# Kernel optimization log

Measured on AMD Instinct MI355X. Metric: run time of the kernel, lower is better.

## Reference

```python
import jax, jax.numpy as jnp
import numpy as np

BANDS = 6
WIN = 10
STRIDE = 2
EPS_LOG = 1e-6


def _radial_masks(win, bands):
    lin = jnp.linspace(-1.0, 1.0, win)
    yy, xx = jnp.meshgrid(lin, lin, indexing='ij')
    rr = jnp.sqrt(xx * xx + yy * yy)
    rr = rr / jnp.maximum(rr.max(), 1e-6)
    edges = jnp.linspace(0.0, 1.0, bands + 1)
    masks = ((rr[None] >= edges[:-1, None, None]) & (rr[None] < edges[1:, None, None])).astype(jnp.float32)
    counts = jnp.maximum(masks.sum(axis=(-2, -1)), 1.0)  # (bands,)
    return masks, counts


def setup_inputs() -> dict:
    key = jax.random.key(0)
    x = jax.random.normal(key, (32, 3, 256, 256), dtype=jnp.float32)
    return {"x": x}


def reference(x):
    # RGB -> gray (B,1,H,W)
    gray = 0.2989 * x[:, 0:1] + 0.587 * x[:, 1:2] + 0.114 * x[:, 2:3]
    patches = jax.lax.conv_general_dilated_patches(
        gray, (WIN, WIN), (STRIDE, STRIDE), 'VALID')
    B = patches.shape[0]
    Ho, Wo = patches.shape[2], patches.shape[3]
    p = patches.reshape(B, WIN, WIN, Ho, Wo)  # (B, wy, wx, Ho, Wo)
    # Per-patch 2D FFT (ortho), fftshift, magnitude
    amp = jnp.abs(jnp.fft.fftshift(jnp.fft.fft2(p, axes=(1, 2), norm='ortho'), axes=(1, 2)))
    masks, counts = _radial_masks(WIN, BANDS)
    # One fused contraction over all bands instead of per-band masked passes
    stat = jnp.einsum('byxhw,kyx->bkhw', amp, masks) / counts[None, :, None, None]
    return jnp.log10(stat + EPS_LOG)  # (B, bands, Ho, Wo)
```

## Files before the change

kernel.cpp:

```cpp
#include <hip/hip_runtime.h>

#define HO 124
#define WO 124

typedef float f2 __attribute__((ext_vector_type(2)));
static __device__ __forceinline__ f2 fma2(f2 a, f2 b, f2 c) {
  return __builtin_elementwise_fma(a, b, c);
}
#define FSQRT(x) __builtin_amdgcn_sqrtf(x)
#define FLOG10(x) (0.30102999566398120f * __builtin_amdgcn_logf(x))

constexpr float K1 = 0.80901699437494745f;
constexpr float K2 = 0.30901699437494742f;
constexpr float G1 = 0.58778525229247314f;
constexpr float G2 = 0.95105651629515357f;

struct Tbl { float v[360]; };
constexpr Tbl mk_wv() {
  Tbl t{};
  int band[100] = {};
  int cnt[6] = {0, 0, 0, 0, 0, 0};
  for (int i = 0; i < 10; ++i)
    for (int j = 0; j < 10; ++j) {
      const int u = (2 * i - 9) < 0 ? (9 - 2 * i) : (2 * i - 9);
      const int v = (2 * j - 9) < 0 ? (9 - 2 * j) : (2 * j - 9);
      const int m = 2 * (u * u + v * v);
      int b = -1;
      for (int k = 0; k < 6; ++k)
        if (m >= 9 * k * k && m < 9 * (k + 1) * (k + 1)) b = k;
      if (u == 3 && v == 3) b = (i == 6 && j == 6) ? 2 : 1;
      if (m == 324) b = 5;
      band[i * 10 + j] = b;
      if (b >= 0) cnt[b]++;
    }
  for (int ky = 0; ky < 6; ++ky)
    for (int kx = 0; kx < 10; ++kx)
      for (int b = 0; b < 6; ++b) {
        float w = 0.0f;
        const int sp = ((ky + 5) % 10) * 10 + (kx + 5) % 10;
        if (band[sp] == b) w += 0.1f / (float)cnt[b];
        if (ky >= 1 && ky <= 4) {
          const int sp2 = ((15 - ky) % 10) * 10 + (15 - kx) % 10;
          if (band[sp2] == b) w += 0.1f / (float)cnt[b];
        }
        t.v[(ky * 10 + kx) * 6 + b] = w;
      }
  return t;
}
constexpr Tbl WVT = mk_wv();

template <int CELL, int B>
struct AccwStep {
  static __device__ __forceinline__ void run(const float amp, float* acc) {
    constexpr float w = WVT.v[CELL * 6 + B];
    if constexpr (w != 0.0f) acc[B] = fmaf(amp, w, acc[B]);
    AccwStep<CELL, B + 1>::run(amp, acc);
  }
};
template <int CELL>
struct AccwStep<CELL, 6> {
  static __device__ __forceinline__ void run(const float, float*) {}
};
template <int C1, int C2, int B>
struct Accw2Step {
  static __device__ __forceinline__ void run(const float amp, float* acc) {
    constexpr float w = WVT.v[C1 * 6 + B] + WVT.v[C2 * 6 + B];
    if constexpr (w != 0.0f) acc[B] = fmaf(amp, w, acc[B]);
    Accw2Step<C1, C2, B + 1>::run(amp, acc);
  }
};
template <int C1, int C2>
struct Accw2Step<C1, C2, 6> {
  static __device__ __forceinline__ void run(const float, float*) {}
};
#define ACCW(cell, amp) AccwStep<(cell), 0>::run((amp), acc)
#define ACCW2(c1, c2, amp) Accw2Step<(c1), (c2), 0>::run((amp), acc)

template <int KY>
__device__ __forceinline__ void plane_body(const f2* __restrict__ tbc,
                                           float* acc) {
  f2 T_[10];
#pragma unroll
  for (int q = 0; q < 10; ++q) T_[q] = tbc[q];
  const f2 EE = T_[0] + T_[5], FF = T_[0] - T_[5];
  const f2 PQ1 = T_[1] + T_[9], MN1 = T_[1] - T_[9];
  const f2 PQ2 = T_[2] + T_[8], MN2 = T_[2] - T_[8];
  const f2 PQ3 = T_[3] + T_[7], MN3 = T_[3] - T_[7];
  const f2 PQ4 = T_[4] + T_[6], MN4 = T_[4] - T_[6];
  const f2 UU1 = PQ1 - PQ4, UU2 = PQ2 - PQ3;
  const f2 VV1 = PQ1 + PQ4, VV2 = PQ2 + PQ3;
  const f2 WW1 = MN1 + MN4, WW2 = MN2 + MN3;
  const f2 ZZ1 = MN1 - MN4, ZZ2 = MN2 - MN3;
  {
    const f2 AC = EE + VV1 + VV2;
    ACCW(KY * 10 + 0, FSQRT(fmaf(AC.x, AC.x, AC.y * AC.y)));
  }
  {
    const f2 AC = FF - UU1 + UU2;
    ACCW(KY * 10 + 5, FSQRT(fmaf(AC.x, AC.x, AC.y * AC.y)));
  }
#define CPLX_PAIR(kx, AC_, DB_)                                         \
  {                                                                     \
    const f2 AC = (AC_);                                                \
    const f2 DB = (DB_);                                                \
    {                                                                   \
      const float fr = AC.x + DB.y, fi = AC.y - DB.x;                   \
      ACCW(KY * 10 + (kx), FSQRT(fmaf(fr, fr, fi * fi)));               \
    }                                                                   \
    {                                                                   \
      const float fr = AC.x - DB.y, fi = AC.y + DB.x;                   \
      ACCW(KY * 10 + 10 - (kx), FSQRT(fmaf(fr, fr, fi * fi)));          \
    }                                                                   \
  }
  CPLX_PAIR(1,
            fma2(UU1, (f2){K1, K1}, fma2(UU2, (f2){K2, K2}, FF)),
            fma2(WW1, (f2){G1, G1}, WW2 * (f2){G2, G2}));
  CPLX_PAIR(2,
            fma2(VV1, (f2){K2, K2}, fma2(VV2, (f2){-K1, -K1}, EE)),
            fma2(ZZ1, (f2){G2, G2}, ZZ2 * (f2){G1, G1}));
  CPLX_PAIR(3,
            fma2(UU1, (f2){-K2, -K2}, fma2(UU2, (f2){-K1, -K1}, FF)),
            fma2(WW1, (f2){G2, G2}, WW2 * (f2){-G1, -G1}));
  CPLX_PAIR(4,
            fma2(VV1, (f2){-K1, -K1}, fma2(VV2, (f2){K2, K2}, EE)),
            fma2(ZZ1, (f2){G1, G1}, ZZ2 * (f2){-G2, -G2}));
#undef CPLX_PAIR
}

__global__ __launch_bounds__(256, 5) void lfs_main(const float* __restrict__ x,
                                                   float* __restrict__ out) {
  __shared__ __attribute__((aligned(16))) float tile[40 * 40];
  __shared__ __attribute__((aligned(16))) f2 Tcp[4 * 16 * 40];
  __shared__ __attribute__((aligned(16))) f2 Trr2[16 * 40];
  const int tid = threadIdx.x;
  const int bx = blockIdx.x, by = blockIdx.y, bb = blockIdx.z;

  const int oy0 = by * 32, ox0 = bx * 32;
  const float* xr = x + (size_t)bb * 3 * 65536;
  const float* xg = xr + 65536;
  const float* xb = xr + 131072;
  const bool xfull = (bx < 7);
  {
    const int r0 = tid / 10, c0 = tid % 10;
    const int gy0 = oy0 + r0;
    const bool p1 = (tid < 144);
    const int t1 = tid + 256;
    const int r1 = t1 / 10, c1 = t1 % 10;
    const int gy1 = oy0 + r1;
    float4 a0 = make_float4(0.f, 0.f, 0.f, 0.f), b0 = a0, d0 = a0;
    float4 a1 = make_float4(0.f, 0.f, 0.f, 0.f), b1 = a1, d1 = a1;
    if (gy0 < 256 && (c0 < 8 || xfull)) {
      const int off = gy0 * 256 + ox0 + c0 * 4;
      a0 = *reinterpret_cast<const float4*>(xr + off);
      b0 = *reinterpret_cast<const float4*>(xg + off);
      d0 = *reinterpret_cast<const float4*>(xb + off);
    }
    if (p1 && gy1 < 256 && (c1 < 8 || xfull)) {
      const int off = gy1 * 256 + ox0 + c1 * 4;
      a1 = *reinterpret_cast<const float4*>(xr + off);
      b1 = *reinterpret_cast<const float4*>(xg + off);
      d1 = *reinterpret_cast<const float4*>(xb + off);
    }
    float4 g0, g1;
    g0.x = fmaf(0.2989f, a0.x, fmaf(0.587f, b0.x, 0.114f * d0.x));
    g0.y = fmaf(0.2989f, a0.y, fmaf(0.587f, b0.y, 0.114f * d0.y));
    g0.z = fmaf(0.2989f, a0.z, fmaf(0.587f, b0.z, 0.114f * d0.z));
    g0.w = fmaf(0.2989f, a0.w, fmaf(0.587f, b0.w, 0.114f * d0.w));
    g1.x = fmaf(0.2989f, a1.x, fmaf(0.587f, b1.x, 0.114f * d1.x));
    g1.y = fmaf(0.2989f, a1.y, fmaf(0.587f, b1.y, 0.114f * d1.y));
    g1.z = fmaf(0.2989f, a1.z, fmaf(0.587f, b1.z, 0.114f * d1.z));
    g1.w = fmaf(0.2989f, a1.w, fmaf(0.587f, b1.w, 0.114f * d1.w));
    *reinterpret_cast<float4*>(&tile[r0 * 40 + c0 * 4]) = g0;
    if (p1) *reinterpret_cast<float4*>(&tile[r1 * 40 + c1 * 4]) = g1;
  }
  __syncthreads();

  for (int a = tid; a < 320; a += 256) {
    const int r = a / 20, cp = a % 20;
    const float* tb0 = &tile[(2 * r) * 40 + 2 * cp];
    f2 col[10];
#pragma unroll
    for (int y = 0; y < 10; ++y)
      col[y] = *reinterpret_cast<const f2*>(&tb0[y * 40]);
    const f2 E = col[0] + col[5], F = col[0] - col[5];
    const f2 P1 = col[1] + col[9], M1 = col[1] - col[9];
    const f2 P2 = col[2] + col[8], M2 = col[2] - col[8];
    const f2 P3 = col[3] + col[7], M3 = col[3] - col[7];
    const f2 P4 = col[4] + col[6], M4 = col[4] - col[6];
    const f2 U1 = P1 - P4, U2 = P2 - P3;
    const f2 V1 = P1 + P4, V2 = P2 + P3;
    const f2 W1 = M1 + M4, W2 = M2 + M3;
    const f2 Z1 = M1 - M4, Z2 = M2 - M3;
    const f2 k0 = E + V1 + V2, k5 = F - U1 + U2;
    const f2 sr1 = fma2(U1, (f2){K1, K1}, fma2(U2, (f2){K2, K2}, F));
    const f2 si1 = fma2(W1, (f2){-G1, -G1}, W2 * (f2){-G2, -G2});
    const f2 sr2 = fma2(V1, (f2){K2, K2}, fma2(V2, (f2){-K1, -K1}, E));
    const f2 si2 = fma2(Z1, (f2){-G2, -G2}, Z2 * (f2){-G1, -G1});
    const f2 sr3 = fma2(U1, (f2){-K2, -K2}, fma2(U2, (f2){-K1, -K1}, F));
    const f2 si3 = fma2(W1, (f2){-G2, -G2}, W2 * (f2){G1, G1});
    const f2 sr4 = fma2(V1, (f2){-K1, -K1}, fma2(V2, (f2){K2, K2}, E));
    const f2 si4 = fma2(Z1, (f2){-G1, -G1}, Z2 * (f2){G2, G2});
    *reinterpret_cast<float4*>(&Trr2[r * 40 + 2 * cp]) =
        make_float4(k0.x, k5.x, k0.y, k5.y);
    *reinterpret_cast<float4*>(&Tcp[(0 * 16 + r) * 40 + 2 * cp]) =
        make_float4(sr1.x, si1.x, sr1.y, si1.y);
    *reinterpret_cast<float4*>(&Tcp[(1 * 16 + r) * 40 + 2 * cp]) =
        make_float4(sr2.x, si2.x, sr2.y, si2.y);
    *reinterpret_cast<float4*>(&Tcp[(2 * 16 + r) * 40 + 2 * cp]) =
        make_float4(sr3.x, si3.x, sr3.y, si3.y);
    *reinterpret_cast<float4*>(&Tcp[(3 * 16 + r) * 40 + 2 * cp]) =
        make_float4(sr4.x, si4.x, sr4.y, si4.y);
  }
  __syncthreads();

  const int tx = tid & 15, ty = tid >> 4;
  const int h = by * 16 + ty, w = bx * 16 + tx;
  const bool valid = (h < HO) && (w < WO);

  if (valid) {
    float acc[6] = {0.f, 0.f, 0.f, 0.f, 0.f, 0.f};

    {
      const f2* tbr = &Trr2[ty * 40 + 2 * tx];
      f2 T_[10];
#pragma unroll
      for (int q = 0; q < 10; ++q) T_[q] = tbr[q];
      const f2 E = T_[0] + T_[5], F = T_[0] - T_[5];
      const f2 P1 = T_[1] + T_[9], M1 = T_[1] - T_[9];
      const f2 P2 = T_[2] + T_[8], M2 = T_[2] - T_[8];
      const f2 P3 = T_[3] + T_[7], M3 = T_[3] - T_[7];
      const f2 P4 = T_[4] + T_[6], M4 = T_[4] - T_[6];
      const f2 U1 = P1 - P4, U2 = P2 - P3;
      const f2 V1 = P1 + P4, V2 = P2 + P3;
      const f2 W1 = M1 + M4, W2 = M2 + M3;
      const f2 Z1 = M1 - M4, Z2 = M2 - M3;
      {
        const f2 A = E + V1 + V2;
        ACCW(0, fabsf(A.x));
        ACCW(50, fabsf(A.y));
      }
      {
        const f2 A = F - U1 + U2;
        ACCW(5, fabsf(A.x));
        ACCW(55, fabsf(A.y));
      }
      {
        const f2 A = fma2((f2){K1, K1}, U1, fma2((f2){K2, K2}, U2, F));
        const f2 D = fma2((f2){G1, G1}, W1, (f2){G2, G2} * W2);
        const f2 s = fma2(A, A, D * D);
        ACCW2(1, 9, FSQRT(s.x));
        ACCW2(51, 59, FSQRT(s.y));
      }
      {
        const f2 A = fma2((f2){K2, K2}, V1, fma2((f2){-K1, -K1}, V2, E));
        const f2 D = fma2((f2){G2, G2}, Z1, (f2){G1, G1} * Z2);
        const f2 s = fma2(A, A, D * D);
        ACCW2(2, 8, FSQRT(s.x));
        ACCW2(52, 58, FSQRT(s.y));
      }
      {
        const f2 A = fma2((f2){-K2, -K2}, U1, fma2((f2){-K1, -K1}, U2, F));
        const f2 D = fma2((f2){G2, G2}, W1, (f2){-G1, -G1} * W2);
        const f2 s = fma2(A, A, D * D);
        ACCW2(3, 7, FSQRT(s.x));
        ACCW2(53, 57, FSQRT(s.y));
      }
      {
        const f2 A = fma2((f2){-K1, -K1}, V1, fma2((f2){K2, K2}, V2, E));
        const f2 D = fma2((f2){G1, G1}, Z1, (f2){-G2, -G2} * Z2);
        const f2 s = fma2(A, A, D * D);
        ACCW2(4, 6, FSQRT(s.x));
        ACCW2(54, 56, FSQRT(s.y));
      }
    }

    plane_body<1>(&Tcp[(0 * 16 + ty) * 40 + 2 * tx], acc);
    plane_body<2>(&Tcp[(1 * 16 + ty) * 40 + 2 * tx], acc);
    plane_body<3>(&Tcp[(2 * 16 + ty) * 40 + 2 * tx], acc);
    plane_body<4>(&Tcp[(3 * 16 + ty) * 40 + 2 * tx], acc);

    const size_t ob = ((size_t)bb * 6) * (HO * WO) + (size_t)h * WO + w;
#pragma unroll
    for (int b = 0; b < 6; ++b)
      out[ob + (size_t)b * (HO * WO)] = FLOG10(acc[b] + 1e-6f);
  }
}

extern "C" void kernel_launch(void* const* d_in, const int* in_sizes, int n_in,
                              void* d_out, int out_size, void* d_ws,
                              size_t ws_size, hipStream_t stream) {
  (void)in_sizes; (void)n_in; (void)out_size; (void)d_ws; (void)ws_size;
  const float* x = (const float*)d_in[0];
  float* out = (float*)d_out;
  lfs_main<<<dim3(8, 8, 32), 256, 0, stream>>>(x, out);
}
```

Before: 22.11 us.

## Process two images per block and prefetch second image during first compute

Each block now handles two batch images (bz and bz+16), halving the grid. The global loads for the second image are issued before the first image's radial-band stage runs, so memory latency can overlap with compute. Occupancy hint drops from 5 to 4 blocks per CU to make room for the extra staged registers. The trade-off is fewer blocks to hide latency with and higher register pressure.

```diff
diff --git a/kernel.cpp b/kernel.cpp
--- a/kernel.cpp
+++ b/kernel.cpp
@@ -127,54 +127,63 @@
 #undef CPLX_PAIR
 }
 
-__global__ __launch_bounds__(256, 5) void lfs_main(const float* __restrict__ x,
-                                                   float* __restrict__ out) {
-  __shared__ __attribute__((aligned(16))) float tile[40 * 40];
-  __shared__ __attribute__((aligned(16))) f2 Tcp[4 * 16 * 40];
-  __shared__ __attribute__((aligned(16))) f2 Trr2[16 * 40];
-  const int tid = threadIdx.x;
-  const int bx = blockIdx.x, by = blockIdx.y, bb = blockIdx.z;
-
-  const int oy0 = by * 32, ox0 = bx * 32;
-  const float* xr = x + (size_t)bb * 3 * 65536;
+struct StageRegs {
+  float4 a0, b0, d0, a1, b1, d1;
+};
+
+__device__ __forceinline__ void issue_loads(const int tid, const int bx,
+                                            const int oy0, const int ox0,
+                                            const float* __restrict__ xr,
+                                            StageRegs& s) {
   const float* xg = xr + 65536;
   const float* xb = xr + 131072;
   const bool xfull = (bx < 7);
-  {
-    const int r0 = tid / 10, c0 = tid % 10;
-    const int gy0 = oy0 + r0;
-    const bool p1 = (tid < 144);
-    const int t1 = tid + 256;
-    const int r1 = t1 / 10, c1 = t1 % 10;
-    const int gy1 = oy0 + r1;
-    float4 a0 = make_float4(0.f, 0.f, 0.f, 0.f), b0 = a0, d0 = a0;
-    float4 a1 = make_float4(0.f, 0.f, 0.f, 0.f), b1 = a1, d1 = a1;
-    if (gy0 < 256 && (c0 < 8 || xfull)) {
-      const int off = gy0 * 256 + ox0 + c0 * 4;
-      a0 = *reinterpret_cast<const float4*>(xr + off);
-      b0 = *reinterpret_cast<const float4*>(xg + off);
-      d0 = *reinterpret_cast<const float4*>(xb + off);
-    }
-    if (p1 && gy1 < 256 && (c1 < 8 || xfull)) {
-      const int off = gy1 * 256 + ox0 + c1 * 4;
-      a1 = *reinterpret_cast<const float4*>(xr + off);
-      b1 = *reinterpret_cast<const float4*>(xg + off);
-      d1 = *reinterpret_cast<const float4*>(xb + off);
-    }
-    float4 g0, g1;
-    g0.x = fmaf(0.2989f, a0.x, fmaf(0.587f, b0.x, 0.114f * d0.x));
-    g0.y = fmaf(0.2989f, a0.y, fmaf(0.587f, b0.y, 0.114f * d0.y));
-    g0.z = fmaf(0.2989f, a0.z, fmaf(0.587f, b0.z, 0.114f * d0.z));
-    g0.w = fmaf(0.2989f, a0.w, fmaf(0.587f, b0.w, 0.114f * d0.w));
-    g1.x = fmaf(0.2989f, a1.x, fmaf(0.587f, b1.x, 0.114f * d1.x));
-    g1.y = fmaf(0.2989f, a1.y, fmaf(0.587f, b1.y, 0.114f * d1.y));
-    g1.z = fmaf(0.2989f, a1.z, fmaf(0.587f, b1.z, 0.114f * d1.z));
-    g1.w = fmaf(0.2989f, a1.w, fmaf(0.587f, b1.w, 0.114f * d1.w));
-    *reinterpret_cast<float4*>(&tile[r0 * 40 + c0 * 4]) = g0;
-    if (p1) *reinterpret_cast<float4*>(&tile[r1 * 40 + c1 * 4]) = g1;
-  }
-  __syncthreads();
-
+  const int r0 = tid / 10, c0 = tid % 10;
+  const int gy0 = oy0 + r0;
+  const bool p1 = (tid < 144);
+  const int t1 = tid + 256;
+  const int r1 = t1 / 10, c1 = t1 % 10;
+  const int gy1 = oy0 + r1;
+  s.a0 = make_float4(0.f, 0.f, 0.f, 0.f);
+  s.b0 = s.a0; s.d0 = s.a0; s.a1 = s.a0; s.b1 = s.a0; s.d1 = s.a0;
+  if (gy0 < 256 && (c0 < 8 || xfull)) {
+    const int off = gy0 * 256 + ox0 + c0 * 4;
+    s.a0 = *reinterpret_cast<const float4*>(xr + off);
+    s.b0 = *reinterpret_cast<const float4*>(xg + off);
+    s.d0 = *reinterpret_cast<const float4*>(xb + off);
+  }
+  if (p1 && gy1 < 256 && (c1 < 8 || xfull)) {
+    const int off = gy1 * 256 + ox0 + c1 * 4;
+    s.a1 = *reinterpret_cast<const float4*>(xr + off);
+    s.b1 = *reinterpret_cast<const float4*>(xg + off);
+    s.d1 = *reinterpret_cast<const float4*>(xb + off);
+  }
+}
+
+__device__ __forceinline__ void conv_store(const int tid,
+                                           float* __restrict__ tile,
+                                           const StageRegs& s) {
+  const int r0 = tid / 10, c0 = tid % 10;
+  const bool p1 = (tid < 144);
+  const int t1 = tid + 256;
+  const int r1 = t1 / 10, c1 = t1 % 10;
+  float4 g0, g1;
+  g0.x = fmaf(0.2989f, s.a0.x, fmaf(0.587f, s.b0.x, 0.114f * s.d0.x));
+  g0.y = fmaf(0.2989f, s.a0.y, fmaf(0.587f, s.b0.y, 0.114f * s.d0.y));
+  g0.z = fmaf(0.2989f, s.a0.z, fmaf(0.587f, s.b0.z, 0.114f * s.d0.z));
+  g0.w = fmaf(0.2989f, s.a0.w, fmaf(0.587f, s.b0.w, 0.114f * s.d0.w));
+  g1.x = fmaf(0.2989f, s.a1.x, fmaf(0.587f, s.b1.x, 0.114f * s.d1.x));
+  g1.y = fmaf(0.2989f, s.a1.y, fmaf(0.587f, s.b1.y, 0.114f * s.d1.y));
+  g1.z = fmaf(0.2989f, s.a1.z, fmaf(0.587f, s.b1.z, 0.114f * s.d1.z));
+  g1.w = fmaf(0.2989f, s.a1.w, fmaf(0.587f, s.b1.w, 0.114f * s.d1.w));
+  *reinterpret_cast<float4*>(&tile[r0 * 40 + c0 * 4]) = g0;
+  if (p1) *reinterpret_cast<float4*>(&tile[r1 * 40 + c1 * 4]) = g1;
+}
+
+__device__ __forceinline__ void stage1_run(const int tid,
+                                           const float* __restrict__ tile,
+                                           f2* __restrict__ Tcp,
+                                           f2* __restrict__ Trr2) {
   for (int a = tid; a < 320; a += 256) {
     const int r = a / 20, cp = a % 20;
     const float* tb0 = &tile[(2 * r) * 40 + 2 * cp];
@@ -211,13 +220,16 @@
     *reinterpret_cast<float4*>(&Tcp[(3 * 16 + r) * 40 + 2 * cp]) =
         make_float4(sr4.x, si4.x, sr4.y, si4.y);
   }
-  __syncthreads();
-
+}
+
+__device__ __forceinline__ void stage2_run(const int tid, const int bx,
+                                           const int by, const int bb,
+                                           const f2* __restrict__ Tcp,
+                                           const f2* __restrict__ Trr2,
+                                           float* __restrict__ out) {
   const int tx = tid & 15, ty = tid >> 4;
   const int h = by * 16 + ty, w = bx * 16 + tx;
-  const bool valid = (h < HO) && (w < WO);
-
-  if (valid) {
+  if ((h < HO) && (w < WO)) {
     float acc[6] = {0.f, 0.f, 0.f, 0.f, 0.f, 0.f};
 
     {
@@ -286,11 +298,42 @@
   }
 }
 
+__global__ __launch_bounds__(256, 4) void lfs_main(const float* __restrict__ x,
+                                                   float* __restrict__ out) {
+  __shared__ __attribute__((aligned(16))) float tile[40 * 40];
+  __shared__ __attribute__((aligned(16))) f2 Tcp[4 * 16 * 40];
+  __shared__ __attribute__((aligned(16))) f2 Trr2[16 * 40];
+  const int tid = threadIdx.x;
+  const int bx = blockIdx.x, by = blockIdx.y, bz = blockIdx.z;
+  const int bb0 = bz, bb1 = bz + 16;
+  const int oy0 = by * 32, ox0 = bx * 32;
+
+  {
+    StageRegs s;
+    issue_loads(tid, bx, oy0, ox0, x + (size_t)bb0 * 3 * 65536, s);
+    conv_store(tid, tile, s);
+  }
+  __syncthreads();
+  stage1_run(tid, tile, Tcp, Trr2);
+  __syncthreads();
+
+  StageRegs s1;
+  issue_loads(tid, bx, oy0, ox0, x + (size_t)bb1 * 3 * 65536, s1);
+
+  stage2_run(tid, bx, by, bb0, Tcp, Trr2, out);
+
+  conv_store(tid, tile, s1);
+  __syncthreads();
+  stage1_run(tid, tile, Tcp, Trr2);
+  __syncthreads();
+  stage2_run(tid, bx, by, bb1, Tcp, Trr2, out);
+}
+
 extern "C" void kernel_launch(void* const* d_in, const int* in_sizes, int n_in,
                               void* d_out, int out_size, void* d_ws,
                               size_t ws_size, hipStream_t stream) {
   (void)in_sizes; (void)n_in; (void)out_size; (void)d_ws; (void)ws_size;
   const float* x = (const float*)d_in[0];
   float* out = (float*)d_out;
-  lfs_main<<<dim3(8, 8, 32), 256, 0, stream>>>(x, out);
-}
+  lfs_main<<<dim3(8, 8, 16), 256, 0, stream>>>(x, out);
+}
```

After: 22.59 us. +2.2%, slower.
